# Optimization experiments

Hardware: AMD Instinct MI355X
Metric: run time of the kernel (lower is better)

Reference implementation:

```python
import jax, jax.numpy as jnp
import numpy as np

N, E, F, H, C = 100000, 3200000, 128, 256, 47
EPS = 1e-5


def setup_inputs() -> dict:
    key = jax.random.key(0)
    ks = jax.random.split(key, 12)
    x = jax.random.normal(ks[0], (N, F), dtype=jnp.float32)
    edge_index = jax.random.randint(ks[1], (2, E), 0, N, dtype=jnp.int64)
    relations = jax.random.randint(ks[2], (E,), 0, 4, dtype=jnp.int64)
    def lin(k, fan_in, fan_out):
        return jax.random.normal(k, (fan_in, fan_out), dtype=jnp.float32) / np.sqrt(fan_in)
    W0 = lin(ks[3], F, H); b0 = jnp.zeros((H,), jnp.float32)
    W1 = lin(ks[4], H, H); b1 = jnp.zeros((H,), jnp.float32)
    W2 = lin(ks[5], H, C); b2 = jnp.zeros((C,), jnp.float32)
    g0 = jnp.ones((H,), jnp.float32); be0 = jnp.zeros((H,), jnp.float32)
    g1 = jnp.ones((H,), jnp.float32); be1 = jnp.zeros((H,), jnp.float32)
    return {"x": x, "edge_index": edge_index, "relations": relations,
            "W0": W0, "b0": b0, "g0": g0, "be0": be0,
            "W1": W1, "b1": b1, "g1": g1, "be1": be1,
            "W2": W2, "b2": b2}


def _gcn_conv(x, W, b, src, dst, n_nodes):
    # GCNConv: linear transform, add self-loops, symmetric degree normalization,
    # gather-scale-scatter aggregation, bias add.
    h = x @ W  # [N, out]
    self_loop = jnp.arange(n_nodes, dtype=src.dtype)
    s = jnp.concatenate([src, self_loop])
    d = jnp.concatenate([dst, self_loop])
    deg = jax.ops.segment_sum(jnp.ones(d.shape[0], h.dtype), d, num_segments=n_nodes)
    dinv = jnp.where(deg > 0, jax.lax.rsqrt(deg), 0.0)
    coef = dinv[s] * dinv[d]  # [E+N]
    out = jax.ops.segment_sum(h[s] * coef[:, None], d, num_segments=n_nodes)
    return out + b


def _batch_norm(x, gamma, beta):
    mean = jnp.mean(x, axis=0)
    var = jnp.var(x, axis=0)
    return (x - mean) * jax.lax.rsqrt(var + EPS) * gamma + beta


def reference(x, edge_index, relations, W0, b0, g0, be0, W1, b1, g1, be1, W2, b2):
    src, dst = edge_index[0], edge_index[1]
    n = x.shape[0]
    h = _gcn_conv(x, W0, b0, src, dst, n)
    h = jax.nn.relu(_batch_norm(h, g0, be0))  # dropout is identity in eval
    h = _gcn_conv(h, W1, b1, src, dst, n)
    h = jax.nn.relu(_batch_norm(h, g1, be1))
    h = _gcn_conv(h, W2, b2, src, dst, n)
    return jax.nn.log_softmax(h, axis=-1)
```

## Files before the change

kernel.cpp:

```cpp
#include <hip/hip_runtime.h>
#include <hip/hip_fp8.h>
#include <math.h>

#define NN 100000
#define NE 3200000
#define FIN 128
#define HD 256
#define CO 47
#define COP 48
#define NBKT 196
#define G 1024
#define CHUNK 3125

typedef _Float16 h2 __attribute__((ext_vector_type(2)));
typedef _Float16 h4 __attribute__((ext_vector_type(4)));
typedef _Float16 h8 __attribute__((ext_vector_type(8)));
typedef float f32x2 __attribute__((ext_vector_type(2)));
typedef float f32x4 __attribute__((ext_vector_type(4)));


__global__ __launch_bounds__(256) void hist_kernel(const int* __restrict__ dst,
                                                   int* __restrict__ hist) {
    __shared__ int h[NBKT];
    int tid = threadIdx.x;
    for (int i = tid; i < NBKT; i += 256) h[i] = 0;
    __syncthreads();
    int base = blockIdx.x * CHUNK;
    for (int i = tid; i < CHUNK; i += 256)
        atomicAdd(&h[dst[base + i] >> 9], 1);
    __syncthreads();
    for (int i = tid; i < NBKT; i += 256) hist[i * G + blockIdx.x] = h[i];
}

__global__ void scan1_kernel(const int* __restrict__ in, int* __restrict__ out,
                             int* __restrict__ bsum, int n) {
    __shared__ int tmp[256];
    int t = threadIdx.x;
    int i = blockIdx.x * 256 + t;
    int v = (i < n) ? in[i] : 0;
    tmp[t] = v;
    __syncthreads();
    #pragma unroll
    for (int off = 1; off < 256; off <<= 1) {
        int u = (t >= off) ? tmp[t - off] : 0;
        __syncthreads();
        tmp[t] += u;
        __syncthreads();
    }
    if (i < n) out[i] = tmp[t] - v;
    if (t == 255) bsum[blockIdx.x] = tmp[255];
}

__global__ void scan2_kernel(int* __restrict__ bsum, int nb) {
    __shared__ int tmp[1024];
    int t = threadIdx.x;
    int v = (t < nb) ? bsum[t] : 0;
    tmp[t] = v;
    __syncthreads();
    #pragma unroll
    for (int off = 1; off < 1024; off <<= 1) {
        int u = (t >= off) ? tmp[t - off] : 0;
        __syncthreads();
        tmp[t] += u;
        __syncthreads();
    }
    if (t < nb) bsum[t] = tmp[t] - v;
    if (t == nb - 1) bsum[nb] = tmp[t];
}

__global__ void scan3_kernel(int* __restrict__ out, const int* __restrict__ bsum,
                             int nb, int n) {
    int i = blockIdx.x * 256 + threadIdx.x;
    if (i < n) out[i] += bsum[i >> 8];
    if (i == 0) out[n] = bsum[nb];
}

__global__ __launch_bounds__(256) void scatter_kernel(const int* __restrict__ src,
                                                      const int* __restrict__ dst,
                                                      const int* __restrict__ hscan,
                                                      int* __restrict__ epk) {
    __shared__ int cur[NBKT];
    int tid = threadIdx.x;
    for (int i = tid; i < NBKT; i += 256) cur[i] = hscan[i * G + blockIdx.x];
    __syncthreads();
    int base = blockIdx.x * CHUNK;
    for (int i = tid; i < CHUNK; i += 256) {
        int e = base + i;
        int d = dst[e];
        int slot = atomicAdd(&cur[d >> 9], 1);
        epk[slot] = ((d & 511) << 17) | src[e];
    }
}

__global__ __launch_bounds__(256) void bucket_fill_kernel(
    const int* __restrict__ hscan, const int* __restrict__ epk,
    int* __restrict__ csr, int* __restrict__ offs, float* __restrict__ dinv)
{
    __shared__ int deg[512], cur[512], a0[512], a1[512];
    int tid = threadIdx.x, b = blockIdx.x;
    int ebeg = hscan[b * G], eend = hscan[(b + 1) * G];
    deg[tid] = 0; deg[tid + 256] = 0;
    __syncthreads();
    for (int e = ebeg + tid; e < eend; e += 256)
        atomicAdd(&deg[((unsigned)epk[e]) >> 17], 1);
    __syncthreads();
    a0[tid] = deg[tid]; a0[tid + 256] = deg[tid + 256];
    __syncthreads();
    int* pin = a0; int* pout = a1;
    for (int off = 1; off < 512; off <<= 1) {
        #pragma unroll
        for (int q = 0; q < 2; ++q) {
            int p = tid + q * 256;
            pout[p] = pin[p] + ((p >= off) ? pin[p - off] : 0);
        }
        __syncthreads();
        int* t = pin; pin = pout; pout = t;
    }
    #pragma unroll
    for (int q = 0; q < 2; ++q) {
        int i = tid + q * 256;
        int excl = pin[i] - deg[i];
        cur[i] = excl;
        int node = b * 512 + i;
        if (node < NN) {
            offs[node] = ebeg + excl;
            dinv[node] = rsqrtf((float)deg[i] + 1.0f);
        }
    }
    if (b == 0 && tid == 0) offs[NN] = NE;
    __syncthreads();
    for (int e = ebeg + tid; e < eend; e += 256) {
        int pk = epk[e];
        int p = atomicAdd(&cur[((unsigned)pk) >> 17], 1);
        csr[ebeg + p] = pk & 0x1FFFF;
    }
}


template<int K>
__global__ void wtrans_kernel(const float* __restrict__ W, _Float16* __restrict__ Wt,
                              int N, int NP) {
    int i = blockIdx.x * 256 + threadIdx.x;
    if (i >= NP * K) return;
    int n = i / K, k = i % K;
    float v = (n < N) ? W[(size_t)k * N + n] : 0.0f;
    Wt[i] = (_Float16)v;
}


__global__ void conv_x_kernel(const float* __restrict__ x, const float* __restrict__ dinv,
                              unsigned* __restrict__ xq) {
    int i = blockIdx.x * 256 + threadIdx.x;
    if (i >= NN * FIN / 4) return;
    int r = i >> 5;
    float4 v = ((const float4*)x)[i];
    float dv = dinv[r];
    int u = __builtin_amdgcn_cvt_pk_fp8_f32(v.x * dv, v.y * dv, 0, false);
    u = __builtin_amdgcn_cvt_pk_fp8_f32(v.z * dv, v.w * dv, u, true);
    xq[i] = (unsigned)u;
}


__global__ __launch_bounds__(256) void agg128_kernel(
    const unsigned short* __restrict__ xq, const int* __restrict__ offs,
    const int* __restrict__ csr, const float* __restrict__ dinv,
    _Float16* __restrict__ out)
{
    int lane = threadIdx.x & 63;
    int v = blockIdx.x * 4 + (threadIdx.x >> 6);
    unsigned sv = xq[(size_t)v * 64 + lane];
    f32x2 acc = __builtin_amdgcn_cvt_pk_f32_fp8((int)sv, false);
    int b = offs[v], e = offs[v + 1], j = b;
    int s[8];
    if (j + 8 <= e) {
        #pragma unroll
        for (int q = 0; q < 8; ++q) s[q] = csr[j + q];
    }
    for (; j + 8 <= e; ) {
        int nj = j + 8;
        int ns[8];
        if (nj + 8 <= e) {
            #pragma unroll
            for (int q = 0; q < 8; ++q) ns[q] = csr[nj + q];
        }
        #pragma unroll
        for (int q = 0; q < 8; ++q) {
            unsigned t = xq[(size_t)s[q] * 64 + lane];
            acc += __builtin_amdgcn_cvt_pk_f32_fp8((int)t, false);
        }
        #pragma unroll
        for (int q = 0; q < 8; ++q) s[q] = ns[q];
        j = nj;
    }
    for (; j < e; ++j) {
        unsigned t = xq[(size_t)csr[j] * 64 + lane];
        acc += __builtin_amdgcn_cvt_pk_f32_fp8((int)t, false);
    }
    float dv = dinv[v];
    h2 o; o[0] = (_Float16)(acc[0] * dv); o[1] = (_Float16)(acc[1] * dv);
    ((h2*)out)[(size_t)v * 64 + lane] = o;
}

__global__ __launch_bounds__(256) void agg256_kernel(
    const unsigned* __restrict__ t1q, const int* __restrict__ offs,
    const int* __restrict__ csr, const float* __restrict__ dinv,
    _Float16* __restrict__ out)
{
    int lane = threadIdx.x & 63;
    int v = blockIdx.x * 4 + (threadIdx.x >> 6);
    unsigned sv = t1q[(size_t)v * 64 + lane];
    f32x2 acc01 = __builtin_amdgcn_cvt_pk_f32_fp8((int)sv, false);
    f32x2 acc23 = __builtin_amdgcn_cvt_pk_f32_fp8((int)sv, true);
    int b = offs[v], e = offs[v + 1], j = b;
    int s[8];
    if (j + 8 <= e) {
        #pragma unroll
        for (int q = 0; q < 8; ++q) s[q] = csr[j + q];
    }
    for (; j + 8 <= e; ) {
        int nj = j + 8;
        int ns[8];
        if (nj + 8 <= e) {
            #pragma unroll
            for (int q = 0; q < 8; ++q) ns[q] = csr[nj + q];
        }
        #pragma unroll
        for (int q = 0; q < 8; ++q) {
            unsigned t = t1q[(size_t)s[q] * 64 + lane];
            acc01 += __builtin_amdgcn_cvt_pk_f32_fp8((int)t, false);
            acc23 += __builtin_amdgcn_cvt_pk_f32_fp8((int)t, true);
        }
        #pragma unroll
        for (int q = 0; q < 8; ++q) s[q] = ns[q];
        j = nj;
    }
    for (; j < e; ++j) {
        unsigned t = t1q[(size_t)csr[j] * 64 + lane];
        acc01 += __builtin_amdgcn_cvt_pk_f32_fp8((int)t, false);
        acc23 += __builtin_amdgcn_cvt_pk_f32_fp8((int)t, true);
    }
    float dv = dinv[v];
    h4 o; o[0] = (_Float16)(acc01[0] * dv); o[1] = (_Float16)(acc01[1] * dv);
    o[2] = (_Float16)(acc23[0] * dv); o[3] = (_Float16)(acc23[1] * dv);
    ((h4*)out)[(size_t)v * 64 + lane] = o;
}

__global__ __launch_bounds__(256) void agg47_lsm_kernel(
    const _Float16* __restrict__ t2, const int* __restrict__ offs,
    const int* __restrict__ csr, const float* __restrict__ dinv,
    const float* __restrict__ bias, float* __restrict__ out)
{
    int lane = threadIdx.x & 63;
    int v = blockIdx.x * 4 + (threadIdx.x >> 6);
    bool act = lane < CO;
    float acc = act ? (float)t2[(size_t)v * COP + lane] : 0.0f;
    int b = offs[v], e = offs[v + 1], j = b;
    int s[8];
    if (j + 8 <= e) {
        #pragma unroll
        for (int q = 0; q < 8; ++q) s[q] = csr[j + q];
    }
    for (; j + 8 <= e; ) {
        int nj = j + 8;
        int ns[8];
        if (nj + 8 <= e) {
            #pragma unroll
            for (int q = 0; q < 8; ++q) ns[q] = csr[nj + q];
        }
        if (act) {
            #pragma unroll
            for (int q = 0; q < 8; ++q) acc += (float)t2[(size_t)s[q] * COP + lane];
        }
        #pragma unroll
        for (int q = 0; q < 8; ++q) s[q] = ns[q];
        j = nj;
    }
    for (; j < e; ++j) if (act) acc += (float)t2[(size_t)csr[j] * COP + lane];
    float val = act ? fmaf(acc, dinv[v], bias[lane]) : -1e30f;
    float m = val;
    #pragma unroll
    for (int o = 32; o > 0; o >>= 1) m = fmaxf(m, __shfl_xor(m, o, 64));
    float ex = act ? expf(val - m) : 0.0f;
    float sum = ex;
    #pragma unroll
    for (int o = 32; o > 0; o >>= 1) sum += __shfl_xor(sum, o, 64);
    if (act) out[(size_t)v * CO + lane] = val - m - logf(sum);
}


#define LDS_PAD 8

template<int K, bool XFORM, bool EPI_DINV, bool OUT8>
__global__ __launch_bounds__(256) void mfma_gemm_big(
    const _Float16* __restrict__ A, int lda,
    const _Float16* __restrict__ Wt,
    const float* __restrict__ ss, const float* __restrict__ dinv,
    void* __restrict__ outp, int ldo)
{
    __shared__ __align__(16) _Float16 As[128][64 + LDS_PAD];
    __shared__ __align__(16) _Float16 Bs[128][64 + LDS_PAD];
    __shared__ float SS[2 * K];
    const int row0 = blockIdx.x * 128;
    const int col0 = blockIdx.y * 128;
    const int tid = threadIdx.x;
    if (XFORM) {
        for (int i = tid; i < 2 * K; i += 256) SS[i] = ss[i];
    }
    const int lane = tid & 63;
    const int wv = tid >> 6;
    const int wr = wv >> 1, wc = wv & 1;
    const int fr = lane & 15;
    const int kb = (lane >> 4) * 8;

    f32x4 acc[4][4];
    #pragma unroll
    for (int m = 0; m < 4; ++m)
        #pragma unroll
        for (int n = 0; n < 4; ++n)
            acc[m][n] = (f32x4){0.f, 0.f, 0.f, 0.f};

    if (XFORM) __syncthreads();

    for (int k0 = 0; k0 < K; k0 += 64) {
        #pragma unroll
        for (int p = 0; p < 4; ++p) {
            int c = p * 256 + tid;
            int m = c >> 3, kk = (c & 7) * 8;
            int r = row0 + m;
            h8 av = {};
            if (r < NN) av = *(const h8*)&A[(size_t)r * lda + k0 + kk];
            if (XFORM) {
                #pragma unroll
                for (int j = 0; j < 8; ++j) {
                    float a = (float)av[j];
                    a = fmaxf(fmaf(a, SS[k0 + kk + j], SS[K + k0 + kk + j]), 0.0f);
                    av[j] = (_Float16)a;
                }
            }
            *(h8*)&As[m][kk] = av;
        }
        #pragma unroll
        for (int p = 0; p < 4; ++p) {
            int c = p * 256 + tid;
            int n = c >> 3, kk = (c & 7) * 8;
            h8 bv = *(const h8*)&Wt[(size_t)(col0 + n) * K + k0 + kk];
            *(h8*)&Bs[n][kk] = bv;
        }
        __syncthreads();
        #pragma unroll
        for (int ks = 0; ks < 2; ++ks) {
            h8 a[4], b[4];
            #pragma unroll
            for (int m = 0; m < 4; ++m)
                a[m] = *(const h8*)&As[wr * 64 + m * 16 + fr][ks * 32 + kb];
            #pragma unroll
            for (int n = 0; n < 4; ++n)
                b[n] = *(const h8*)&Bs[wc * 64 + n * 16 + fr][ks * 32 + kb];
            #pragma unroll
            for (int m = 0; m < 4; ++m)
                #pragma unroll
                for (int n = 0; n < 4; ++n)
                    acc[m][n] = __builtin_amdgcn_mfma_f32_16x16x32_f16(a[m], b[n], acc[m][n], 0, 0, 0);
        }
        __syncthreads();
    }

    const int fq = lane >> 4;
    #pragma unroll
    for (int m = 0; m < 4; ++m) {
        #pragma unroll
        for (int j = 0; j < 4; ++j) {
            int r = row0 + wr * 64 + m * 16 + fq * 4 + j;
            if (r >= NN) continue;
            float dv = EPI_DINV ? dinv[r] : 1.0f;
            #pragma unroll
            for (int n = 0; n < 4; n += 2) {
                int c0 = col0 + wc * 64 + n * 16 + fr;
                int c1 = c0 + 16;
                float v0 = acc[m][n][j] * dv;
                float v1 = acc[m][n + 1][j] * dv;
                if (OUT8) {
                    int pk = __builtin_amdgcn_cvt_pk_fp8_f32(v0, v1, 0, false);
                    ((unsigned char*)outp)[(size_t)r * ldo + c0] = (unsigned char)(pk & 0xFF);
                    ((unsigned char*)outp)[(size_t)r * ldo + c1] = (unsigned char)((pk >> 8) & 0xFF);
                } else {
                    ((_Float16*)outp)[(size_t)r * ldo + c0] = (_Float16)v0;
                    ((_Float16*)outp)[(size_t)r * ldo + c1] = (_Float16)v1;
                }
            }
        }
    }
}


template<int K, bool XFORM, bool EPI_DINV>
__global__ __launch_bounds__(256) void mfma_gemm_kernel(
    const _Float16* __restrict__ A, int lda,
    const _Float16* __restrict__ Wt,
    const float* __restrict__ ss, const float* __restrict__ dinv,
    _Float16* __restrict__ out, int ldo, int ncolsO)
{
    __shared__ __align__(16) _Float16 As[128][32 + LDS_PAD];
    __shared__ __align__(16) _Float16 Bs[64][32 + LDS_PAD];
    __shared__ float SS[2 * K];
    const int row0 = blockIdx.x * 128;
    const int col0 = blockIdx.y * 64;
    const int tid = threadIdx.x;
    if (XFORM) {
        for (int i = tid; i < 2 * K; i += 256) SS[i] = ss[i];
    }
    const int lane = tid & 63;
    const int wv = tid >> 6;
    const int wr = wv >> 1, wc = wv & 1;
    const int fr = lane & 15;
    const int kb = (lane >> 4) * 8;

    f32x4 acc[4][2];
    #pragma unroll
    for (int m = 0; m < 4; ++m)
        #pragma unroll
        for (int n = 0; n < 2; ++n)
            acc[m][n] = (f32x4){0.f, 0.f, 0.f, 0.f};

    if (XFORM) __syncthreads();

    for (int k0 = 0; k0 < K; k0 += 32) {
        #pragma unroll
        for (int p = 0; p < 2; ++p) {
            int idx = (p * 256 + tid) * 8;
            int m = idx >> 5, kk = idx & 31;
            int r = row0 + m;
            h8 av = {};
            if (r < NN) av = *(const h8*)&A[(size_t)r * lda + k0 + kk];
            if (XFORM) {
                #pragma unroll
                for (int j = 0; j < 8; ++j) {
                    float a = (float)av[j];
                    a = fmaxf(fmaf(a, SS[k0 + kk + j], SS[K + k0 + kk + j]), 0.0f);
                    av[j] = (_Float16)a;
                }
            }
            *(h8*)&As[m][kk] = av;
        }
        {
            int idx = tid * 8;
            int n = idx >> 5, kk = idx & 31;
            h8 bv = *(const h8*)&Wt[(size_t)(col0 + n) * K + k0 + kk];
            *(h8*)&Bs[n][kk] = bv;
        }
        __syncthreads();
        h8 a[4], b[2];
        #pragma unroll
        for (int m = 0; m < 4; ++m)
            a[m] = *(const h8*)&As[wr * 64 + m * 16 + fr][kb];
        #pragma unroll
        for (int n = 0; n < 2; ++n)
            b[n] = *(const h8*)&Bs[wc * 32 + n * 16 + fr][kb];
        #pragma unroll
        for (int m = 0; m < 4; ++m)
            #pragma unroll
            for (int n = 0; n < 2; ++n)
                acc[m][n] = __builtin_amdgcn_mfma_f32_16x16x32_f16(a[m], b[n], acc[m][n], 0, 0, 0);
        __syncthreads();
    }

    const int fq = lane >> 4;
    #pragma unroll
    for (int m = 0; m < 4; ++m) {
        #pragma unroll
        for (int j = 0; j < 4; ++j) {
            int r = row0 + wr * 64 + m * 16 + fq * 4 + j;
            if (r >= NN) continue;
            float dv = EPI_DINV ? dinv[r] : 1.0f;
            #pragma unroll
            for (int n = 0; n < 2; ++n) {
                int c = col0 + wc * 32 + n * 16 + fr;
                if (c < ncolsO) out[(size_t)r * ldo + c] = (_Float16)(acc[m][n][j] * dv);
            }
        }
    }
}


__global__ __launch_bounds__(256) void bn_part_kernel(const _Float16* __restrict__ h,
                                                      float* __restrict__ part) {
    int tid = threadIdx.x;
    int fg = tid & 63;
    int rg = tid >> 6;
    float s1[4] = {}, s2[4] = {};
    for (int r = blockIdx.x * 4 + rg; r < NN; r += 4096) {
        h4 v = ((const h4*)(h + (size_t)r * HD))[fg];
        #pragma unroll
        for (int j = 0; j < 4; ++j) {
            float f = (float)v[j];
            s1[j] += f; s2[j] += f * f;
        }
    }
    __shared__ float sm[256][8];
    #pragma unroll
    for (int j = 0; j < 4; ++j) { sm[tid][j] = s1[j]; sm[tid][4 + j] = s2[j]; }
    __syncthreads();
    if (tid < 64) {
        float o1[4] = {}, o2[4] = {};
        #pragma unroll
        for (int r = 0; r < 4; ++r)
            #pragma unroll
            for (int j = 0; j < 4; ++j) {
                o1[j] += sm[r * 64 + tid][j];
                o2[j] += sm[r * 64 + tid][4 + j];
            }
        #pragma unroll
        for (int j = 0; j < 4; ++j) {
            part[(size_t)blockIdx.x * 512 + tid * 4 + j] = o1[j];
            part[(size_t)blockIdx.x * 512 + 256 + tid * 4 + j] = o2[j];
        }
    }
}

__global__ __launch_bounds__(256) void bn_reduce_kernel(const float* __restrict__ part,
                                                        const float* __restrict__ g,
                                                        const float* __restrict__ be,
                                                        float* __restrict__ ss) {
    int f = blockIdx.x * 32 + (threadIdx.x & 31);
    int c = threadIdx.x >> 5;
    float s1 = 0.f, s2 = 0.f;
    for (int b = c; b < 1024; b += 8) {
        s1 += part[(size_t)b * 512 + f];
        s2 += part[(size_t)b * 512 + 256 + f];
    }
    __shared__ float m1[8][32], m2[8][32];
    m1[c][threadIdx.x & 31] = s1; m2[c][threadIdx.x & 31] = s2;
    __syncthreads();
    if (threadIdx.x < 32) {
        float t1 = 0.f, t2 = 0.f;
        #pragma unroll
        for (int q = 0; q < 8; ++q) { t1 += m1[q][threadIdx.x]; t2 += m2[q][threadIdx.x]; }
        float mean = t1 * (1.0f / NN);
        float var = t2 * (1.0f / NN) - mean * mean;
        float sc = g[f] * rsqrtf(var + 1e-5f);
        ss[f] = sc;
        ss[HD + f] = be[f] - mean * sc;
    }
}


extern "C" void kernel_launch(void* const* d_in, const int* in_sizes, int n_in,
                              void* d_out, int out_size, void* d_ws, size_t ws_size,
                              hipStream_t stream) {
    const float* x   = (const float*)d_in[0];
    const int*   ei  = (const int*)d_in[1];
    const float* W0  = (const float*)d_in[3];
    const float* g0  = (const float*)d_in[5];
    const float* be0 = (const float*)d_in[6];
    const float* W1  = (const float*)d_in[7];
    const float* g1  = (const float*)d_in[9];
    const float* be1 = (const float*)d_in[10];
    const float* W2  = (const float*)d_in[11];
    const float* b2  = (const float*)d_in[12];
    float* out = (float*)d_out;

    const int* src = ei;
    const int* dst = ei + NE;

    const size_t S = 51200000;
    char* ws = (char*)d_ws;
    unsigned*  xq  = (unsigned*)ws;
    unsigned*  t1q = (unsigned*)ws;
    _Float16*  t2  = (_Float16*)ws;
    _Float16*  a0  = (_Float16*)(ws + 25600000);
    _Float16*  S2  = (_Float16*)(ws + S);
    char* base2 = ws + 2 * S;
    int*   csr  = (int*)  (base2);
    int*   offs = (int*)  (base2 + 12800000);
    float* dinv = (float*)(base2 + 13200064);
    float* ssb  = (float*)(base2 + 13602112);
    int*   bsum = (int*)  (base2 + 13604160);
    _Float16* wt0 = (_Float16*)(base2 + 13608320);
    _Float16* wt1 = (_Float16*)(base2 + 13673856);
    _Float16* wt2 = (_Float16*)(base2 + 13804928);
    int*   hist = (int*)  (base2 + 13837696);
    int*   epk  = (int*)  (base2 + 14640576);
    float* part = (float*)(base2 + 27440576);

    const int N2 = NBKT * G;
    const int NB2 = (N2 + 255) / 256;
    hist_kernel<<<G, 256, 0, stream>>>(dst, hist);
    scan1_kernel<<<NB2, 256, 0, stream>>>(hist, hist, bsum, N2);
    scan2_kernel<<<1, 1024, 0, stream>>>(bsum, NB2);
    scan3_kernel<<<NB2, 256, 0, stream>>>(hist, bsum, NB2, N2);
    scatter_kernel<<<G, 256, 0, stream>>>(src, dst, hist, epk);
    bucket_fill_kernel<<<NBKT, 256, 0, stream>>>(hist, epk, csr, offs, dinv);

    wtrans_kernel<FIN><<<(256 * FIN + 255) / 256, 256, 0, stream>>>(W0, wt0, HD, HD);
    wtrans_kernel<HD><<<(256 * HD + 255) / 256, 256, 0, stream>>>(W1, wt1, HD, HD);
    wtrans_kernel<HD><<<(64 * HD + 255) / 256, 256, 0, stream>>>(W2, wt2, CO, 64);

    const int MB = (NN + 127) / 128;

    conv_x_kernel<<<(NN * FIN / 4 + 255) / 256, 256, 0, stream>>>(x, dinv, xq);
    agg128_kernel<<<NN / 4, 256, 0, stream>>>((const unsigned short*)xq, offs, csr, dinv, a0);
    mfma_gemm_big<FIN, false, false, false><<<dim3(MB, 2), 256, 0, stream>>>(
        a0, FIN, wt0, nullptr, dinv, S2, HD);

    bn_part_kernel<<<1024, 256, 0, stream>>>(S2, part);
    bn_reduce_kernel<<<8, 256, 0, stream>>>(part, g0, be0, ssb);

    mfma_gemm_big<HD, true, true, true><<<dim3(MB, 2), 256, 0, stream>>>(
        S2, HD, wt1, ssb, dinv, t1q, HD);
    agg256_kernel<<<NN / 4, 256, 0, stream>>>(t1q, offs, csr, dinv, S2);

    bn_part_kernel<<<1024, 256, 0, stream>>>(S2, part);
    bn_reduce_kernel<<<8, 256, 0, stream>>>(part, g1, be1, ssb);

    mfma_gemm_kernel<HD, true, true><<<dim3(MB, 1), 256, 0, stream>>>(
        S2, HD, wt2, ssb, dinv, t2, COP, CO);
    agg47_lsm_kernel<<<NN / 4, 256, 0, stream>>>(t2, offs, csr, dinv, b2, out);
}
```

Before: 591.6 us.

## Restructure histogram scan, stage fp8 GEMM epilogue in LDS, deepen gather prefetch

The three-pass global scan over the bucket histogram becomes a per-bucket row scan plus a small scan of bucket totals, and those totals are added to the offsets in scatter and bucket_fill. The fp8 GEMM epilogue now stages its output tile in LDS and writes 16-byte coalesced rows instead of scattered byte stores. The 256-wide aggregation prefetches 16 neighbour indices per step instead of 8. The GEMM grid is flattened so the two column tiles of a row block run in adjacent blocks, aiming at better L2 reuse of A. The changes cut launches and uncoalesced traffic but raise register pressure in the aggregation kernel.

```diff
diff --git a/kernel.cpp b/kernel.cpp
--- a/kernel.cpp
+++ b/kernel.cpp
@@ -17,6 +17,7 @@
 typedef _Float16 h8 __attribute__((ext_vector_type(8)));
 typedef float f32x2 __attribute__((ext_vector_type(2)));
 typedef float f32x4 __attribute__((ext_vector_type(4)));
+typedef unsigned int u32x4 __attribute__((ext_vector_type(4)));
 
 
 __global__ __launch_bounds__(256) void hist_kernel(const int* __restrict__ dst,
@@ -32,12 +33,34 @@
     for (int i = tid; i < NBKT; i += 256) hist[i * G + blockIdx.x] = h[i];
 }
 
-__global__ void scan1_kernel(const int* __restrict__ in, int* __restrict__ out,
-                             int* __restrict__ bsum, int n) {
+__global__ __launch_bounds__(256) void rowscan_kernel(int* __restrict__ hist,
+                                                      int* __restrict__ btot) {
+    __shared__ int sums[256];
+    int b = blockIdx.x, t = threadIdx.x;
+    int base = b * G + t * 4;
+    int4 v = *(int4*)&hist[base];
+    int i0 = v.x, i1 = i0 + v.y, i2 = i1 + v.z, i3 = i2 + v.w;
+    sums[t] = i3;
+    __syncthreads();
+    #pragma unroll
+    for (int off = 1; off < 256; off <<= 1) {
+        int u = (t >= off) ? sums[t - off] : 0;
+        __syncthreads();
+        sums[t] += u;
+        __syncthreads();
+    }
+    int excl = sums[t] - i3;
+    hist[base] = excl;
+    hist[base + 1] = excl + i0;
+    hist[base + 2] = excl + i1;
+    hist[base + 3] = excl + i2;
+    if (t == 255) btot[b] = sums[255];
+}
+
+__global__ void totscan_kernel(const int* __restrict__ btot, int* __restrict__ bbase) {
     __shared__ int tmp[256];
     int t = threadIdx.x;
-    int i = blockIdx.x * 256 + t;
-    int v = (i < n) ? in[i] : 0;
+    int v = (t < NBKT) ? btot[t] : 0;
     tmp[t] = v;
     __syncthreads();
     #pragma unroll
@@ -47,41 +70,19 @@
         tmp[t] += u;
         __syncthreads();
     }
-    if (i < n) out[i] = tmp[t] - v;
-    if (t == 255) bsum[blockIdx.x] = tmp[255];
-}
-
-__global__ void scan2_kernel(int* __restrict__ bsum, int nb) {
-    __shared__ int tmp[1024];
-    int t = threadIdx.x;
-    int v = (t < nb) ? bsum[t] : 0;
-    tmp[t] = v;
-    __syncthreads();
-    #pragma unroll
-    for (int off = 1; off < 1024; off <<= 1) {
-        int u = (t >= off) ? tmp[t - off] : 0;
-        __syncthreads();
-        tmp[t] += u;
-        __syncthreads();
-    }
-    if (t < nb) bsum[t] = tmp[t] - v;
-    if (t == nb - 1) bsum[nb] = tmp[t];
-}
-
-__global__ void scan3_kernel(int* __restrict__ out, const int* __restrict__ bsum,
-                             int nb, int n) {
-    int i = blockIdx.x * 256 + threadIdx.x;
-    if (i < n) out[i] += bsum[i >> 8];
-    if (i == 0) out[n] = bsum[nb];
+    if (t < NBKT) bbase[t] = tmp[t] - v;
+    if (t == NBKT - 1) bbase[NBKT] = tmp[t];
 }
 
 __global__ __launch_bounds__(256) void scatter_kernel(const int* __restrict__ src,
                                                       const int* __restrict__ dst,
                                                       const int* __restrict__ hscan,
+                                                      const int* __restrict__ bbase,
                                                       int* __restrict__ epk) {
     __shared__ int cur[NBKT];
     int tid = threadIdx.x;
-    for (int i = tid; i < NBKT; i += 256) cur[i] = hscan[i * G + blockIdx.x];
+    for (int i = tid; i < NBKT; i += 256)
+        cur[i] = hscan[i * G + blockIdx.x] + bbase[i];
     __syncthreads();
     int base = blockIdx.x * CHUNK;
     for (int i = tid; i < CHUNK; i += 256) {
@@ -93,12 +94,12 @@
 }
 
 __global__ __launch_bounds__(256) void bucket_fill_kernel(
-    const int* __restrict__ hscan, const int* __restrict__ epk,
+    const int* __restrict__ bbase, const int* __restrict__ epk,
     int* __restrict__ csr, int* __restrict__ offs, float* __restrict__ dinv)
 {
     __shared__ int deg[512], cur[512], a0[512], a1[512];
     int tid = threadIdx.x, b = blockIdx.x;
-    int ebeg = hscan[b * G], eend = hscan[(b + 1) * G];
+    int ebeg = bbase[b], eend = bbase[b + 1];
     deg[tid] = 0; deg[tid + 256] = 0;
     __syncthreads();
     for (int e = ebeg + tid; e < eend; e += 256)
@@ -212,26 +213,26 @@
     f32x2 acc01 = __builtin_amdgcn_cvt_pk_f32_fp8((int)sv, false);
     f32x2 acc23 = __builtin_amdgcn_cvt_pk_f32_fp8((int)sv, true);
     int b = offs[v], e = offs[v + 1], j = b;
-    int s[8];
-    if (j + 8 <= e) {
-        #pragma unroll
-        for (int q = 0; q < 8; ++q) s[q] = csr[j + q];
-    }
-    for (; j + 8 <= e; ) {
-        int nj = j + 8;
-        int ns[8];
-        if (nj + 8 <= e) {
-            #pragma unroll
-            for (int q = 0; q < 8; ++q) ns[q] = csr[nj + q];
-        }
-        #pragma unroll
-        for (int q = 0; q < 8; ++q) {
+    int s[16];
+    if (j + 16 <= e) {
+        #pragma unroll
+        for (int q = 0; q < 16; ++q) s[q] = csr[j + q];
+    }
+    for (; j + 16 <= e; ) {
+        int nj = j + 16;
+        int ns[16];
+        if (nj + 16 <= e) {
+            #pragma unroll
+            for (int q = 0; q < 16; ++q) ns[q] = csr[nj + q];
+        }
+        #pragma unroll
+        for (int q = 0; q < 16; ++q) {
             unsigned t = t1q[(size_t)s[q] * 64 + lane];
             acc01 += __builtin_amdgcn_cvt_pk_f32_fp8((int)t, false);
             acc23 += __builtin_amdgcn_cvt_pk_f32_fp8((int)t, true);
         }
         #pragma unroll
-        for (int q = 0; q < 8; ++q) s[q] = ns[q];
+        for (int q = 0; q < 16; ++q) s[q] = ns[q];
         j = nj;
     }
     for (; j < e; ++j) {
@@ -300,8 +301,8 @@
     __shared__ __align__(16) _Float16 As[128][64 + LDS_PAD];
     __shared__ __align__(16) _Float16 Bs[128][64 + LDS_PAD];
     __shared__ float SS[2 * K];
-    const int row0 = blockIdx.x * 128;
-    const int col0 = blockIdx.y * 128;
+    const int row0 = (blockIdx.x >> 1) * 128;
+    const int col0 = (blockIdx.x & 1) * 128;
     const int tid = threadIdx.x;
     if (XFORM) {
         for (int i = tid; i < 2 * K; i += 256) SS[i] = ss[i];
@@ -366,26 +367,48 @@
     }
 
     const int fq = lane >> 4;
-    #pragma unroll
-    for (int m = 0; m < 4; ++m) {
-        #pragma unroll
-        for (int j = 0; j < 4; ++j) {
-            int r = row0 + wr * 64 + m * 16 + fq * 4 + j;
-            if (r >= NN) continue;
-            float dv = EPI_DINV ? dinv[r] : 1.0f;
-            #pragma unroll
-            for (int n = 0; n < 4; n += 2) {
-                int c0 = col0 + wc * 64 + n * 16 + fr;
-                int c1 = c0 + 16;
-                float v0 = acc[m][n][j] * dv;
-                float v1 = acc[m][n + 1][j] * dv;
-                if (OUT8) {
+    if (OUT8) {
+        unsigned char* stg = (unsigned char*)&As[0][0];
+        #pragma unroll
+        for (int m = 0; m < 4; ++m) {
+            #pragma unroll
+            for (int j = 0; j < 4; ++j) {
+                int rr = wr * 64 + m * 16 + fq * 4 + j;
+                int r = row0 + rr;
+                float dv = (EPI_DINV && r < NN) ? dinv[r] : 1.0f;
+                #pragma unroll
+                for (int n = 0; n < 4; n += 2) {
+                    int cc0 = wc * 64 + n * 16 + fr;
+                    float v0 = acc[m][n][j] * dv;
+                    float v1 = acc[m][n + 1][j] * dv;
                     int pk = __builtin_amdgcn_cvt_pk_fp8_f32(v0, v1, 0, false);
-                    ((unsigned char*)outp)[(size_t)r * ldo + c0] = (unsigned char)(pk & 0xFF);
-                    ((unsigned char*)outp)[(size_t)r * ldo + c1] = (unsigned char)((pk >> 8) & 0xFF);
-                } else {
-                    ((_Float16*)outp)[(size_t)r * ldo + c0] = (_Float16)v0;
-                    ((_Float16*)outp)[(size_t)r * ldo + c1] = (_Float16)v1;
+                    stg[rr * 128 + cc0] = (unsigned char)(pk & 0xFF);
+                    stg[rr * 128 + cc0 + 16] = (unsigned char)((pk >> 8) & 0xFF);
+                }
+            }
+        }
+        __syncthreads();
+        #pragma unroll
+        for (int p = 0; p < 4; ++p) {
+            int rr = p * 32 + (tid >> 3);
+            int cc = (tid & 7) * 16;
+            int r = row0 + rr;
+            if (r < NN)
+                *(u32x4*)&((unsigned char*)outp)[(size_t)r * ldo + col0 + cc] =
+                    *(u32x4*)&stg[rr * 128 + cc];
+        }
+    } else {
+        #pragma unroll
+        for (int m = 0; m < 4; ++m) {
+            #pragma unroll
+            for (int j = 0; j < 4; ++j) {
+                int r = row0 + wr * 64 + m * 16 + fq * 4 + j;
+                if (r >= NN) continue;
+                float dv = EPI_DINV ? dinv[r] : 1.0f;
+                #pragma unroll
+                for (int n = 0; n < 4; ++n) {
+                    int c = col0 + wc * 64 + n * 16 + fr;
+                    ((_Float16*)outp)[(size_t)r * ldo + c] = (_Float16)(acc[m][n][j] * dv);
                 }
             }
         }
@@ -574,7 +597,8 @@
     int*   offs = (int*)  (base2 + 12800000);
     float* dinv = (float*)(base2 + 13200064);
     float* ssb  = (float*)(base2 + 13602112);
-    int*   bsum = (int*)  (base2 + 13604160);
+    int*   btot = (int*)  (base2 + 13604160);
+    int*   bbase= (int*)  (base2 + 13605184);
     _Float16* wt0 = (_Float16*)(base2 + 13608320);
     _Float16* wt1 = (_Float16*)(base2 + 13673856);
     _Float16* wt2 = (_Float16*)(base2 + 13804928);
@@ -582,14 +606,11 @@
     int*   epk  = (int*)  (base2 + 14640576);
     float* part = (float*)(base2 + 27440576);
 
-    const int N2 = NBKT * G;
-    const int NB2 = (N2 + 255) / 256;
     hist_kernel<<<G, 256, 0, stream>>>(dst, hist);
-    scan1_kernel<<<NB2, 256, 0, stream>>>(hist, hist, bsum, N2);
-    scan2_kernel<<<1, 1024, 0, stream>>>(bsum, NB2);
-    scan3_kernel<<<NB2, 256, 0, stream>>>(hist, bsum, NB2, N2);
-    scatter_kernel<<<G, 256, 0, stream>>>(src, dst, hist, epk);
-    bucket_fill_kernel<<<NBKT, 256, 0, stream>>>(hist, epk, csr, offs, dinv);
+    rowscan_kernel<<<NBKT, 256, 0, stream>>>(hist, btot);
+    totscan_kernel<<<1, 256, 0, stream>>>(btot, bbase);
+    scatter_kernel<<<G, 256, 0, stream>>>(src, dst, hist, bbase, epk);
+    bucket_fill_kernel<<<NBKT, 256, 0, stream>>>(bbase, epk, csr, offs, dinv);
 
     wtrans_kernel<FIN><<<(256 * FIN + 255) / 256, 256, 0, stream>>>(W0, wt0, HD, HD);
     wtrans_kernel<HD><<<(256 * HD + 255) / 256, 256, 0, stream>>>(W1, wt1, HD, HD);
@@ -599,13 +620,13 @@
 
     conv_x_kernel<<<(NN * FIN / 4 + 255) / 256, 256, 0, stream>>>(x, dinv, xq);
     agg128_kernel<<<NN / 4, 256, 0, stream>>>((const unsigned short*)xq, offs, csr, dinv, a0);
-    mfma_gemm_big<FIN, false, false, false><<<dim3(MB, 2), 256, 0, stream>>>(
+    mfma_gemm_big<FIN, false, false, false><<<MB * 2, 256, 0, stream>>>(
         a0, FIN, wt0, nullptr, dinv, S2, HD);
 
     bn_part_kernel<<<1024, 256, 0, stream>>>(S2, part);
     bn_reduce_kernel<<<8, 256, 0, stream>>>(part, g0, be0, ssb);
 
-    mfma_gemm_big<HD, true, true, true><<<dim3(MB, 2), 256, 0, stream>>>(
+    mfma_gemm_big<HD, true, true, true><<<MB * 2, 256, 0, stream>>>(
         S2, HD, wt1, ssb, dinv, t1q, HD);
     agg256_kernel<<<NN / 4, 256, 0, stream>>>(t1q, offs, csr, dinv, S2);
 
```

New measurement: 643.6 us. +8.8%, slower.
